# Kernel optimization log

Hardware: AMD Instinct MI355X
Metric: run time of the kernel (lower is better)

The kernel has to match this reference:

```python
import jax, jax.numpy as jnp
import numpy as np

K, D, Q, N = 32, 256, 16, 4096
LOG2PI = float(np.log(2.0 * np.pi))


def setup_inputs() -> dict:
    key = jax.random.key(0)
    k1, k2, k3, k4 = jax.random.split(key, 4)
    X = jax.random.normal(k1, (N, D), dtype=jnp.float32)
    log_pi = jnp.full((K,), -np.log(K), dtype=jnp.float32)  # uniform mixture weights
    mu = 0.1 * jax.random.normal(k2, (K, D), dtype=jnp.float32)
    Lambda = 0.1 * jax.random.normal(k3, (K, D, Q), dtype=jnp.float32)
    log_psi = np.float32(np.log(0.01)) + 0.1 * jax.random.normal(k4, (K, D), dtype=jnp.float32)
    return {"X": X, "log_pi": log_pi, "mu": mu, "Lambda": Lambda, "log_psi": log_psi}


def reference(X, log_pi, mu, Lambda, log_psi):
    """MFA e_step: per-component Gaussian log-prob with C_k = L_k L_k^T + diag(psi_k) + jitter.
    Returns (log_resp_norm [N,K], log_likelihood [N]) — same math as the torch loop, batched over K."""
    d = X.shape[1]
    psi = jnp.exp(log_psi) + 1e-6                       # [K,D]
    C = jnp.einsum('kdq,keq->kde', Lambda, Lambda)       # [K,D,D] low-rank part
    C = C + jnp.eye(d, dtype=X.dtype) * (psi + 1e-5)[:, None, :]  # add diag(psi) + 1e-5 jitter
    chol = jnp.linalg.cholesky(C)                        # [K,D,D]
    diff = X[None, :, :] - mu[:, None, :]                # [K,N,D]
    # solve chol @ y = diff^T  (batched lower-triangular solve)
    y = jax.scipy.linalg.solve_triangular(chol, diff.transpose(0, 2, 1), lower=True)  # [K,D,N]
    maha = jnp.sum(y * y, axis=1)                        # [K,N]
    logdet = 2.0 * jnp.sum(jnp.log(jnp.diagonal(chol, axis1=1, axis2=2)), axis=1)  # [K]
    log_prob = -0.5 * (maha + d * LOG2PI + logdet[:, None])  # [K,N]
    log_resps = log_prob.T + log_pi[None, :]             # [N,K]
    log_likelihood = jax.scipy.special.logsumexp(log_resps, axis=1)  # [N]
    log_resp_norm = log_resps - log_likelihood[:, None]
    return log_resp_norm, log_likelihood
```

## Files before the change

### kernel.cpp

```cpp
#include <hip/hip_runtime.h>
#include <math.h>

#define KC 32
#define DD 256
#define QQ 16
#define NPTS 4096
#define NROW 16
#define LOG2PI_F 1.8378770664093453f

typedef unsigned short ushort_t;

#define OFF_U    0
#define OFF_LOGC 512
#define OFF_HB   544

__device__ __forceinline__ ushort_t f2bf(float f) {
    union { float f; unsigned int u; } c; c.f = f;
    unsigned int u = c.u;
    return (ushort_t)((u + 0x7FFFu + ((u >> 16) & 1u)) >> 16);
}
__device__ __forceinline__ float bf2f(ushort_t h) {
    union { unsigned int u; float f; } c; c.u = ((unsigned int)h) << 16;
    return c.f;
}

using short8 = __attribute__((ext_vector_type(8))) short;
using f32x4  = __attribute__((ext_vector_type(4))) float;

#define HSTR 264
__global__ __launch_bounds__(256) void precompute_kernel(
    const float* __restrict__ log_pi, const float* __restrict__ mu,
    const float* __restrict__ Lambda, const float* __restrict__ log_psi,
    float* __restrict__ ws)
{
    __shared__ __align__(16) ushort_t lamH[QQ * HSTR];
    __shared__ __align__(16) ushort_t lhatH[QQ * HSTR];
    __shared__ __align__(16) ushort_t smuH[QQ * HSTR];
    __shared__ float sM[QQ * 17];
    __shared__ float sL[QQ * 17];
    __shared__ float sY[QQ * 17];
    __shared__ float sPart[8];
    __shared__ float sScal[2];

    const int k = blockIdx.x;
    const int tid = threadIdx.x;
    const int lane = tid & 63;
    const int wave = tid >> 6;
    ushort_t* hb = (ushort_t*)(ws + OFF_HB);
    const int d = tid;

    float Psi  = expf(log_psi[k * DD + d]) + 1.1e-5f;
    float vinv = 1.0f / Psi;
    float mud  = mu[k * DD + d];
    float wv   = vinv * mud;
    hb[(512 + k) * DD + d] = f2bf(vinv);
    hb[(544 + k) * DD + d] = f2bf(wv);
    smuH[d] = f2bf(mud);
    float logPsi = logf(Psi);
    float ckp = wv * mud;

    {
        const float4* lrow = reinterpret_cast<const float4*>(Lambda + (size_t)(k * DD + d) * QQ);
#pragma unroll
        for (int i = 0; i < 4; ++i) {
            float4 t = lrow[i];
            float l0 = t.x, l1 = t.y, l2 = t.z, l3 = t.w;
            int q = 4 * i;
            lamH[(q + 0) * HSTR + d] = f2bf(l0);
            lamH[(q + 1) * HSTR + d] = f2bf(l1);
            lamH[(q + 2) * HSTR + d] = f2bf(l2);
            lamH[(q + 3) * HSTR + d] = f2bf(l3);
            ushort_t h0 = f2bf(l0 * vinv), h1 = f2bf(l1 * vinv);
            ushort_t h2 = f2bf(l2 * vinv), h3 = f2bf(l3 * vinv);
            lhatH[(q + 0) * HSTR + d] = h0;
            lhatH[(q + 1) * HSTR + d] = h1;
            lhatH[(q + 2) * HSTR + d] = h2;
            lhatH[(q + 3) * HSTR + d] = h3;
            hb[(k * QQ + q + 0) * DD + d] = h0;
            hb[(k * QQ + q + 1) * DD + d] = h1;
            hb[(k * QQ + q + 2) * DD + d] = h2;
            hb[(k * QQ + q + 3) * DD + d] = h3;
        }
    }
#pragma unroll
    for (int i = 0; i < 4; ++i) {
        int idx = tid + i * 256;
        if (idx < 990)
            *reinterpret_cast<ushort4*>(smuH + HSTR + idx * 4) = make_ushort4(0, 0, 0, 0);
    }

    float r0 = logPsi, r1 = ckp;
#pragma unroll
    for (int off = 32; off >= 1; off >>= 1) {
        r0 += __shfl_down(r0, off);
        r1 += __shfl_down(r1, off);
    }
    if ((tid & 63) == 0) { sPart[wave] = r0; sPart[4 + wave] = r1; }
    __syncthreads();
    if (tid == 0) {
        sScal[0] = sPart[0] + sPart[1] + sPart[2] + sPart[3];
        sScal[1] = sPart[4] + sPart[5] + sPart[6] + sPart[7];
    }

    if (wave == 0) {
        const int arow = lane & 15;
        const int quad = lane >> 4;
        const ushort_t* pa = lhatH + arow * HSTR + quad * 8;
        const ushort_t* pl = lamH  + arow * HSTR + quad * 8;
        const ushort_t* pm = smuH  + arow * HSTR + quad * 8;
        f32x4 accM = (f32x4){0.f, 0.f, 0.f, 0.f};
        f32x4 accU = (f32x4){0.f, 0.f, 0.f, 0.f};
#pragma unroll
        for (int ks = 0; ks < 8; ++ks) {
            short8 a = *reinterpret_cast<const short8*>(pa + ks * 32);
            accM = __builtin_amdgcn_mfma_f32_16x16x32_bf16(
                a, *reinterpret_cast<const short8*>(pl + ks * 32), accM, 0, 0, 0);
            accU = __builtin_amdgcn_mfma_f32_16x16x32_bf16(
                a, *reinterpret_cast<const short8*>(pm + ks * 32), accU, 0, 0, 0);
        }
#pragma unroll
        for (int reg = 0; reg < 4; ++reg) {
            int q = quad * 4 + reg;
            sM[q * 17 + arow] = accM[reg] + ((q == arow) ? 1.0f : 0.0f);
        }
        if (arow == 0) {
#pragma unroll
            for (int reg = 0; reg < 4; ++reg)
                ws[OFF_U + k * QQ + quad * 4 + reg] = accU[reg];
        }

        if (lane < QQ) {
            const int r = lane;
            float m[QQ], l[QQ];
#pragma unroll
            for (int c = 0; c < QQ; ++c) m[c] = sM[r * 17 + c];
#pragma unroll
            for (int j = 0; j < QQ; ++j) {
                float djj = __shfl(m[j], j);
                float rinv = 1.0f / sqrtf(djj);
                l[j] = m[j] * rinv;
                sL[r * 17 + 16] = l[j];
#pragma unroll
                for (int c = 0; c < QQ; ++c)
                    if (c > j) m[c] -= l[j] * sL[c * 17 + 16];
            }
#pragma unroll
            for (int j = 0; j < QQ; ++j) sL[r * 17 + j] = l[j];
            float dl = logf(l[r]);
            dl += __shfl_xor(dl, 1); dl += __shfl_xor(dl, 2);
            dl += __shfl_xor(dl, 4); dl += __shfl_xor(dl, 8);
            if (r == 0) sPart[1] = dl;

            float y[QQ];
#pragma unroll
            for (int j = 0; j < QQ; ++j) {
                float acc = (j == r) ? 1.0f : 0.0f;
#pragma unroll
                for (int i = 0; i < QQ; ++i)
                    if (i < j) acc -= sL[j * 17 + i] * y[i];
                y[j] = acc / sL[j * 17 + j];
            }
#pragma unroll
            for (int j = 0; j < QQ; ++j) sY[j * 17 + r] = y[j];
        }
    }
    __syncthreads();

    {
        int q = tid >> 4, r = tid & 15;
        float acc = 0.f;
#pragma unroll
        for (int j = 0; j < QQ; ++j) acc += sY[j * 17 + q] * sY[j * 17 + r];
        hb[(576 + k) * DD + tid] = f2bf(acc);
    }
    if (tid == 0) {
        float logdet = sScal[0] + 2.0f * sPart[1];
        ws[OFF_LOGC + k] = log_pi[k] - 0.5f * ((float)DD * LOG2PI_F + logdet)
                         - 0.5f * sScal[1];
    }
}

#define SXH 264
#define TSTR 520
#define QSTR 68
#define MSTR 264
#define SRS 36

__global__ __launch_bounds__(512, 2) void main_kernel(
    const float* __restrict__ X, const float* __restrict__ ws,
    float* __restrict__ out)
{
    const int tid  = threadIdx.x;
    const int lane = tid & 63;
    const int wave = tid >> 6;
    const int n0   = blockIdx.x * NROW;
    const ushort_t* hB = (const ushort_t*)(ws + OFF_HB);

    __shared__ __align__(16) ushort_t xh[NROW * SXH];
    __shared__ __align__(16) ushort_t sT[NROW * TSTR];
    __shared__ __align__(16) ushort_t sMin[KC * MSTR];
    __shared__ __align__(16) float    sQS[NROW * QSTR];
    __shared__ float sU[512];
    __shared__ float sLogc[KC];
    __shared__ float sR[NROW * SRS];
    __shared__ float sLse[NROW];

    {
        const float4* gx = reinterpret_cast<const float4*>(X + (size_t)n0 * DD);
#pragma unroll
        for (int i = 0; i < 2; ++i) {
            int f = tid + i * 512;
            int row = f >> 6, d4 = f & 63;
            float4 v = gx[f];
            *reinterpret_cast<ushort4*>(&xh[row * SXH + d4 * 4]) =
                make_ushort4(f2bf(v.x), f2bf(v.y), f2bf(v.z), f2bf(v.w));
        }
#pragma unroll
        for (int i = 0; i < 4; ++i) {
            int f = tid + i * 512;
            int row = f >> 6, c4 = f & 63;
            *reinterpret_cast<ushort4*>(&sMin[row * MSTR + c4 * 4]) =
                *reinterpret_cast<const ushort4*>(hB + (size_t)(576 + row) * DD + c4 * 4);
        }
        sU[tid] = ws[OFF_U + tid];
        if (tid < KC) sLogc[tid] = ws[OFF_LOGC + tid];
    }
    __syncthreads();

    {
        const int arow = lane & 15;
        const int quad = lane >> 4;
        short8 a[8];
        const ushort_t* ab = xh + arow * SXH + quad * 8;
#pragma unroll
        for (int ks = 0; ks < 8; ++ks) a[ks] = *reinterpret_cast<const short8*>(ab + ks * 32);

        short8 b[4][8];
#pragma unroll
        for (int i = 0; i < 4; ++i) {
            const ushort_t* gB = hB + (size_t)((wave * 4 + i) * 16 + arow) * DD + quad * 8;
#pragma unroll
            for (int ks = 0; ks < 8; ++ks)
                b[i][ks] = *reinterpret_cast<const short8*>(gB + ks * 32);
        }
        f32x4 acc[4];
#pragma unroll
        for (int i = 0; i < 4; ++i) acc[i] = (f32x4){0.f, 0.f, 0.f, 0.f};
#pragma unroll
        for (int ks = 0; ks < 8; ++ks)
#pragma unroll
            for (int i = 0; i < 4; ++i)
                acc[i] = __builtin_amdgcn_mfma_f32_16x16x32_bf16(a[ks], b[i][ks], acc[i], 0, 0, 0);
#pragma unroll
        for (int i = 0; i < 4; ++i) {
            const int tile = wave * 4 + i;
            float uu = sU[tile * 16 + arow];
#pragma unroll
            for (int r = 0; r < 4; ++r)
                sT[(quad * 4 + r) * TSTR + tile * 16 + arow] = f2bf(acc[i][r] - uu);
        }
        if (wave < 4) {
            short8 aa[8];
            if (wave < 2) {
#pragma unroll
                for (int ks = 0; ks < 8; ++ks) {
                    short8 sq;
#pragma unroll
                    for (int e = 0; e < 8; ++e) {
                        float xf = bf2f((ushort_t)a[ks][e]);
                        sq[e] = (short)f2bf(xf * xf);
                    }
                    aa[ks] = sq;
                }
            } else {
#pragma unroll
                for (int ks = 0; ks < 8; ++ks) aa[ks] = a[ks];
            }
            const ushort_t* gB = hB + (size_t)(512 + wave * 16 + arow) * DD + quad * 8;
            f32x4 accs = (f32x4){0.f, 0.f, 0.f, 0.f};
#pragma unroll
            for (int ks = 0; ks < 8; ++ks)
                accs = __builtin_amdgcn_mfma_f32_16x16x32_bf16(
                    aa[ks], *reinterpret_cast<const short8*>(gB + ks * 32), accs, 0, 0, 0);
            const int col = (wave & 1) * 16 + arow + ((wave >> 1) & 1) * 32;
#pragma unroll
            for (int r = 0; r < 4; ++r)
                sQS[(quad * 4 + r) * QSTR + col] = accs[r];
        }
    }
    __syncthreads();

    {
        const int half = tid & 1;
        const int row  = (tid >> 1) & 15;
        const int c0   = tid >> 5;
#pragma unroll
        for (int ci = 0; ci < 2; ++ci) {
            const int c = c0 + ci * 16;
            float t[16];
            {
                const ushort_t* tp = sT + row * TSTR + c * 16;
                short8 t0 = *reinterpret_cast<const short8*>(tp);
                short8 t1 = *reinterpret_cast<const short8*>(tp + 8);
#pragma unroll
                for (int e = 0; e < 8; ++e) {
                    t[e]     = bf2f((ushort_t)t0[e]);
                    t[8 + e] = bf2f((ushort_t)t1[e]);
                }
            }
            const ushort_t* mp = sMin + c * MSTR + half * 128;
            float corr = 0.f;
#pragma unroll
            for (int q = 0; q < 8; ++q) {
                short8 m0 = *reinterpret_cast<const short8*>(mp + q * 16);
                short8 m1 = *reinterpret_cast<const short8*>(mp + q * 16 + 8);
                float inner = 0.f;
#pragma unroll
                for (int e = 0; e < 8; ++e)
                    inner += bf2f((ushort_t)m0[e]) * t[e] + bf2f((ushort_t)m1[e]) * t[8 + e];
                corr += t[half * 8 + q] * inner;
            }
            corr += __shfl_xor(corr, 1);
            if (half == 0) {
                float qx = sQS[row * QSTR + c];
                float sx = sQS[row * QSTR + 32 + c];
                sR[row * SRS + c] = sLogc[c] - 0.5f * (qx - 2.0f * sx - corr);
            }
        }
    }
    __syncthreads();

    if (tid < NROW) {
        float m = -INFINITY;
#pragma unroll
        for (int c = 0; c < KC; ++c) m = fmaxf(m, sR[tid * SRS + c]);
        float sum = 0.f;
#pragma unroll
        for (int c = 0; c < KC; ++c) sum += expf(sR[tid * SRS + c] - m);
        float lse = m + logf(sum);
        sLse[tid] = lse;
        out[(size_t)NPTS * KC + n0 + tid] = lse;
    }
    __syncthreads();
    if (tid < NROW * 8) {
        int r = tid >> 3, i = tid & 7;
        float lse = sLse[r];
        float4 v = *reinterpret_cast<const float4*>(sR + r * SRS + i * 4);
        float4 o = make_float4(v.x - lse, v.y - lse, v.z - lse, v.w - lse);
        *reinterpret_cast<float4*>(out + (size_t)(n0 + r) * KC + i * 4) = o;
    }
}

extern "C" void kernel_launch(void* const* d_in, const int* in_sizes, int n_in,
                              void* d_out, int out_size, void* d_ws, size_t ws_size,
                              hipStream_t stream)
{
    (void)in_sizes; (void)n_in; (void)out_size; (void)ws_size;
    const float* X       = (const float*)d_in[0];
    const float* log_pi  = (const float*)d_in[1];
    const float* mu      = (const float*)d_in[2];
    const float* Lambda  = (const float*)d_in[3];
    const float* log_psi = (const float*)d_in[4];
    float* out = (float*)d_out;
    float* ws  = (float*)d_ws;

    precompute_kernel<<<dim3(KC), dim3(256), 0, stream>>>(log_pi, mu, Lambda, log_psi, ws);
    main_kernel<<<dim3(NPTS / NROW), dim3(512), 0, stream>>>(X, ws, out);
}
```

Baseline: 84.27 us.

## Fold Cholesky factor into projection so Woodbury correction becomes a squared norm

The precompute kernel now multiplies Psi^-1·Lambda by the inverse Cholesky factor of the small Q×Q capacitance matrix and also transforms the offset vector u. The main kernel's Woodbury correction t^T M^-1 t therefore reduces to a sum of squares of the MFMA outputs, computed with in-register xor-shuffle reductions. This drops the Q×Q correction matrix, the bf16 staging of T in shared memory and the per-component quadratic-form loop, which cuts LDS traffic and one compute phase. The MFMA loop is also split into two passes of two tiles each to lower register pressure. The cost is extra shuffles and a slightly different bf16 rounding path.

```diff
diff --git a/kernel.cpp b/kernel.cpp
--- a/kernel.cpp
+++ b/kernel.cpp
@@ -39,6 +39,7 @@
     __shared__ float sM[QQ * 17];
     __shared__ float sL[QQ * 17];
     __shared__ float sY[QQ * 17];
+    __shared__ float sUvec[QQ];
     __shared__ float sPart[8];
     __shared__ float sScal[2];
 
@@ -59,27 +60,19 @@
     float logPsi = logf(Psi);
     float ckp = wv * mud;
 
+    float lam[QQ];
     {
         const float4* lrow = reinterpret_cast<const float4*>(Lambda + (size_t)(k * DD + d) * QQ);
 #pragma unroll
         for (int i = 0; i < 4; ++i) {
             float4 t = lrow[i];
-            float l0 = t.x, l1 = t.y, l2 = t.z, l3 = t.w;
-            int q = 4 * i;
-            lamH[(q + 0) * HSTR + d] = f2bf(l0);
-            lamH[(q + 1) * HSTR + d] = f2bf(l1);
-            lamH[(q + 2) * HSTR + d] = f2bf(l2);
-            lamH[(q + 3) * HSTR + d] = f2bf(l3);
-            ushort_t h0 = f2bf(l0 * vinv), h1 = f2bf(l1 * vinv);
-            ushort_t h2 = f2bf(l2 * vinv), h3 = f2bf(l3 * vinv);
-            lhatH[(q + 0) * HSTR + d] = h0;
-            lhatH[(q + 1) * HSTR + d] = h1;
-            lhatH[(q + 2) * HSTR + d] = h2;
-            lhatH[(q + 3) * HSTR + d] = h3;
-            hb[(k * QQ + q + 0) * DD + d] = h0;
-            hb[(k * QQ + q + 1) * DD + d] = h1;
-            hb[(k * QQ + q + 2) * DD + d] = h2;
-            hb[(k * QQ + q + 3) * DD + d] = h3;
+            lam[4 * i + 0] = t.x; lam[4 * i + 1] = t.y;
+            lam[4 * i + 2] = t.z; lam[4 * i + 3] = t.w;
+        }
+#pragma unroll
+        for (int q = 0; q < QQ; ++q) {
+            lamH[q * HSTR + d]  = f2bf(lam[q]);
+            lhatH[q * HSTR + d] = f2bf(lam[q] * vinv);
         }
     }
 #pragma unroll
@@ -126,7 +119,7 @@
         if (arow == 0) {
 #pragma unroll
             for (int reg = 0; reg < 4; ++reg)
-                ws[OFF_U + k * QQ + quad * 4 + reg] = accU[reg];
+                sUvec[quad * 4 + reg] = accU[reg];
         }
 
         if (lane < QQ) {
@@ -162,16 +155,25 @@
             }
 #pragma unroll
             for (int j = 0; j < QQ; ++j) sY[j * 17 + r] = y[j];
-        }
-    }
-    __syncthreads();
-
-    {
-        int q = tid >> 4, r = tid & 15;
-        float acc = 0.f;
-#pragma unroll
-        for (int j = 0; j < QQ; ++j) acc += sY[j * 17 + q] * sY[j * 17 + r];
-        hb[(576 + k) * DD + tid] = f2bf(acc);
+
+            float u2 = 0.f;
+#pragma unroll
+            for (int i = 0; i < QQ; ++i)
+                u2 += sY[r * 17 + i] * sUvec[i];
+            ws[OFF_U + k * QQ + r] = u2;
+        }
+    }
+    __syncthreads();
+
+    {
+#pragma unroll
+        for (int q = 0; q < QQ; ++q) {
+            float acc = 0.f;
+#pragma unroll
+            for (int j = 0; j < QQ; ++j)
+                acc += lam[j] * sY[q * 17 + j];
+            hb[(k * QQ + q) * DD + d] = f2bf(vinv * acc);
+        }
     }
     if (tid == 0) {
         float logdet = sScal[0] + 2.0f * sPart[1];
@@ -181,9 +183,8 @@
 }
 
 #define SXH 264
-#define TSTR 520
 #define QSTR 68
-#define MSTR 264
+#define CSTR 36
 #define SRS 36
 
 __global__ __launch_bounds__(512, 2) void main_kernel(
@@ -197,9 +198,8 @@
     const ushort_t* hB = (const ushort_t*)(ws + OFF_HB);
 
     __shared__ __align__(16) ushort_t xh[NROW * SXH];
-    __shared__ __align__(16) ushort_t sT[NROW * TSTR];
-    __shared__ __align__(16) ushort_t sMin[KC * MSTR];
     __shared__ __align__(16) float    sQS[NROW * QSTR];
+    __shared__ __align__(16) float    sCorr[NROW * CSTR];
     __shared__ float sU[512];
     __shared__ float sLogc[KC];
     __shared__ float sR[NROW * SRS];
@@ -215,13 +215,6 @@
             *reinterpret_cast<ushort4*>(&xh[row * SXH + d4 * 4]) =
                 make_ushort4(f2bf(v.x), f2bf(v.y), f2bf(v.z), f2bf(v.w));
         }
-#pragma unroll
-        for (int i = 0; i < 4; ++i) {
-            int f = tid + i * 512;
-            int row = f >> 6, c4 = f & 63;
-            *reinterpret_cast<ushort4*>(&sMin[row * MSTR + c4 * 4]) =
-                *reinterpret_cast<const ushort4*>(hB + (size_t)(576 + row) * DD + c4 * 4);
-        }
         sU[tid] = ws[OFF_U + tid];
         if (tid < KC) sLogc[tid] = ws[OFF_LOGC + tid];
     }
@@ -235,29 +228,46 @@
 #pragma unroll
         for (int ks = 0; ks < 8; ++ks) a[ks] = *reinterpret_cast<const short8*>(ab + ks * 32);
 
-        short8 b[4][8];
-#pragma unroll
-        for (int i = 0; i < 4; ++i) {
-            const ushort_t* gB = hB + (size_t)((wave * 4 + i) * 16 + arow) * DD + quad * 8;
+#pragma unroll
+        for (int pass = 0; pass < 2; ++pass) {
+            short8 b[2][8];
+#pragma unroll
+            for (int i = 0; i < 2; ++i) {
+                const int tile = wave * 4 + pass * 2 + i;
+                const ushort_t* gB = hB + (size_t)(tile * 16 + arow) * DD + quad * 8;
+#pragma unroll
+                for (int ks = 0; ks < 8; ++ks)
+                    b[i][ks] = *reinterpret_cast<const short8*>(gB + ks * 32);
+            }
+            f32x4 acc[2];
+#pragma unroll
+            for (int i = 0; i < 2; ++i) acc[i] = (f32x4){0.f, 0.f, 0.f, 0.f};
 #pragma unroll
             for (int ks = 0; ks < 8; ++ks)
-                b[i][ks] = *reinterpret_cast<const short8*>(gB + ks * 32);
-        }
-        f32x4 acc[4];
-#pragma unroll
-        for (int i = 0; i < 4; ++i) acc[i] = (f32x4){0.f, 0.f, 0.f, 0.f};
-#pragma unroll
-        for (int ks = 0; ks < 8; ++ks)
-#pragma unroll
-            for (int i = 0; i < 4; ++i)
-                acc[i] = __builtin_amdgcn_mfma_f32_16x16x32_bf16(a[ks], b[i][ks], acc[i], 0, 0, 0);
-#pragma unroll
-        for (int i = 0; i < 4; ++i) {
-            const int tile = wave * 4 + i;
-            float uu = sU[tile * 16 + arow];
-#pragma unroll
-            for (int r = 0; r < 4; ++r)
-                sT[(quad * 4 + r) * TSTR + tile * 16 + arow] = f2bf(acc[i][r] - uu);
+#pragma unroll
+                for (int i = 0; i < 2; ++i)
+                    acc[i] = __builtin_amdgcn_mfma_f32_16x16x32_bf16(a[ks], b[i][ks], acc[i], 0, 0, 0);
+#pragma unroll
+            for (int i = 0; i < 2; ++i) {
+                const int tile = wave * 4 + pass * 2 + i;
+                float uu = sU[tile * 16 + arow];
+                float s0 = acc[i][0] - uu, s1 = acc[i][1] - uu,
+                      s2 = acc[i][2] - uu, s3 = acc[i][3] - uu;
+                s0 *= s0; s1 *= s1; s2 *= s2; s3 *= s3;
+#pragma unroll
+                for (int mask = 1; mask < 16; mask <<= 1) {
+                    s0 += __shfl_xor(s0, mask);
+                    s1 += __shfl_xor(s1, mask);
+                    s2 += __shfl_xor(s2, mask);
+                    s3 += __shfl_xor(s3, mask);
+                }
+                if (arow == 0) {
+                    sCorr[(quad * 4 + 0) * CSTR + tile] = s0;
+                    sCorr[(quad * 4 + 1) * CSTR + tile] = s1;
+                    sCorr[(quad * 4 + 2) * CSTR + tile] = s2;
+                    sCorr[(quad * 4 + 3) * CSTR + tile] = s3;
+                }
+            }
         }
         if (wave < 4) {
             short8 aa[8];
@@ -291,42 +301,11 @@
     __syncthreads();
 
     {
-        const int half = tid & 1;
-        const int row  = (tid >> 1) & 15;
-        const int c0   = tid >> 5;
-#pragma unroll
-        for (int ci = 0; ci < 2; ++ci) {
-            const int c = c0 + ci * 16;
-            float t[16];
-            {
-                const ushort_t* tp = sT + row * TSTR + c * 16;
-                short8 t0 = *reinterpret_cast<const short8*>(tp);
-                short8 t1 = *reinterpret_cast<const short8*>(tp + 8);
-#pragma unroll
-                for (int e = 0; e < 8; ++e) {
-                    t[e]     = bf2f((ushort_t)t0[e]);
-                    t[8 + e] = bf2f((ushort_t)t1[e]);
-                }
-            }
-            const ushort_t* mp = sMin + c * MSTR + half * 128;
-            float corr = 0.f;
-#pragma unroll
-            for (int q = 0; q < 8; ++q) {
-                short8 m0 = *reinterpret_cast<const short8*>(mp + q * 16);
-                short8 m1 = *reinterpret_cast<const short8*>(mp + q * 16 + 8);
-                float inner = 0.f;
-#pragma unroll
-                for (int e = 0; e < 8; ++e)
-                    inner += bf2f((ushort_t)m0[e]) * t[e] + bf2f((ushort_t)m1[e]) * t[8 + e];
-                corr += t[half * 8 + q] * inner;
-            }
-            corr += __shfl_xor(corr, 1);
-            if (half == 0) {
-                float qx = sQS[row * QSTR + c];
-                float sx = sQS[row * QSTR + 32 + c];
-                sR[row * SRS + c] = sLogc[c] - 0.5f * (qx - 2.0f * sx - corr);
-            }
-        }
+        const int row = tid & 15, c = tid >> 4;
+        float qx   = sQS[row * QSTR + c];
+        float sx   = sQS[row * QSTR + 32 + c];
+        float corr = sCorr[row * CSTR + c];
+        sR[row * SRS + c] = sLogc[c] - 0.5f * (qx - 2.0f * sx - corr);
     }
     __syncthreads();
 
```

Result: faster. 82.08 us (-2.6%).
